# Kernel optimization log

Measured on AMD Instinct MI355X. Metric: run time of the kernel, lower is better.

The kernel has to match this reference:

```python
import jax, jax.numpy as jnp
import numpy as np

NUM_QUBITS = 8
QD = 2 ** NUM_QUBITS          # 256
PI = float(np.pi)
D_MODEL = 512
NUM_HEADS = 8
HEAD_DIM = D_MODEL // NUM_HEADS
LN_EPS = 1e-5


def _superposition(feat):
    # torch bug faithfully reproduced: state starts as e0 and is *multiplied*
    # by per-qubit amplitudes, so only index 0 survives. All values real.
    B, S, d = feat.shape
    idx = np.arange(NUM_QUBITS) % d
    theta = feat[:, :, idx] * PI                       # [B,S,nq]
    cos_h = jnp.cos(theta * 0.5)
    sin_h = jnp.sin(theta * 0.5)
    mask = (np.arange(QD)[None, :] >> np.arange(NUM_QUBITS)[:, None]) & 1  # [nq,QD]
    amps = jnp.where(mask[None, None] == 0, cos_h[..., None], sin_h[..., None])  # [B,S,nq,QD]
    prod = jnp.prod(amps, axis=2)                      # [B,S,QD]
    e0 = jnp.zeros((QD,), feat.dtype).at[0].set(1.0)
    state = prod * e0
    norm = jnp.sqrt(jnp.sum(state * state, axis=-1, keepdims=True))
    return state / (norm + 1e-10)


def _linear_entangle(ent):
    # entangle_matrix is block-diagonal with symmetric 2x2 blocks [[a,a],[a,-a]];
    # state @ M.T == pairwise 2x2 matmul (identical math, avoids 65536^2 matrix)
    B, S, D = ent.shape
    a = 0.7071
    M = jnp.array([[a, a], [a, -a]], ent.dtype)
    return (ent.reshape(B, S, D // 2, 2) @ M).reshape(B, S, D)


def _layer_norm(x, g, b):
    m = jnp.mean(x, axis=-1, keepdims=True)
    v = jnp.mean((x - m) ** 2, axis=-1, keepdims=True)
    return (x - m) * jax.lax.rsqrt(v + LN_EPS) * g + b


def setup_inputs() -> dict:
    key = jax.random.key(0)
    ks = jax.random.split(key, 16)
    D = D_MODEL
    s = 1.0 / np.sqrt(D)
    inp = {
        'audio_features': jax.random.normal(ks[0], (2, 256, D), jnp.float32),
        'visual_features': jax.random.normal(ks[1], (2, 256, D), jnp.float32),
        'Wq': jax.random.normal(ks[2], (D, D), jnp.float32) * s,
        'bq': jnp.zeros((D,), jnp.float32),
        'Wk': jax.random.normal(ks[3], (D, D), jnp.float32) * s,
        'bk': jnp.zeros((D,), jnp.float32),
        'Wv': jax.random.normal(ks[4], (D, D), jnp.float32) * s,
        'bv': jnp.zeros((D,), jnp.float32),
        'Wo': jax.random.normal(ks[5], (D, D), jnp.float32) * s,
        'bo': jnp.zeros((D,), jnp.float32),
        'We': jax.random.normal(ks[6], (D, D), jnp.float32) * s,
        'be': jnp.zeros((D,), jnp.float32),
        'gamma': jnp.ones((D,), jnp.float32),
        'beta': jnp.zeros((D,), jnp.float32),
    }
    return inp


def reference(audio_features, visual_features, Wq, bq, Wk, bk, Wv, bv,
              Wo, bo, We, be, gamma, beta):
    B, S, D = audio_features.shape
    H, hd = NUM_HEADS, HEAD_DIM

    aq = audio_features @ Wq + bq
    av = audio_features @ Wv + bv
    vk = visual_features @ Wk + bk
    vv = visual_features @ Wv + bv

    qa = _superposition(audio_features @ We + be)    # [B,S,QD]
    qv = _superposition(visual_features @ We + be)   # [B,S,QD]
    ent = (qa[..., :, None] * qv[..., None, :]).reshape(B, S, QD * QD)
    ent = _linear_entangle(ent)                      # [B,S,QD^2]

    probs = ent * ent
    qsum = jnp.sum(probs, axis=-1)                   # [B,S]
    ang = jnp.where(ent < 0, PI, 0.0)                # angle of a real number
    interference = jnp.cos(jnp.mean(ang, axis=-1))   # [B,S]
    scale = (qsum * interference)[:, None, :, None]  # [B,1,S,1]

    def heads(x):
        return x.reshape(B, S, H, hd).transpose(0, 2, 1, 3)

    aqh, vkh, vvh, avh = heads(aq), heads(vk), heads(vv), heads(av)
    logits = scale * jnp.einsum('bhqd,bhkd->bhqk', aqh, vkh) / np.sqrt(hd)
    attn = jax.nn.softmax(logits, axis=-1)           # [B,H,S,S]

    audio_att = jnp.einsum('bhqk,bhkd->bhqd', attn, vvh)
    visual_att = jnp.einsum('bhqk,bhqd->bhkd', attn, avh)
    audio_out = audio_att.transpose(0, 2, 1, 3).reshape(B, S, D) @ Wo + bo
    visual_out = visual_att.transpose(0, 2, 1, 3).reshape(B, S, D) @ Wo + bo

    audio_final = _layer_norm(audio_features + audio_out, gamma, beta)
    visual_final = _layer_norm(visual_features + visual_out, gamma, beta)

    quantum_coherence = jnp.mean(jnp.abs(ent))
    pn = probs / (jnp.sum(probs, axis=-1, keepdims=True) + 1e-10)
    entanglement_entropy = jnp.mean(-jnp.sum(pn * jnp.log(pn + 1e-10), axis=-1))

    return (audio_final, visual_final, quantum_coherence,
            entanglement_entropy, attn[:, -1])
```

## Files before the change

kernel.cpp:

```cpp
#include <hip/hip_runtime.h>
#include <math.h>

#define PI_F 3.14159265358979323846f

typedef __attribute__((ext_vector_type(8))) short short8v;
typedef __attribute__((ext_vector_type(4))) float f32x4;
typedef __attribute__((ext_vector_type(16))) float f32x16;

__device__ __forceinline__ unsigned short f2bf(float f) {
    unsigned int u = __float_as_uint(f);
    u += 0x7fffu + ((u >> 16) & 1u);
    return (unsigned short)(u >> 16);
}

__device__ __forceinline__ unsigned int cvtpk_bf16(float lo, float hi) {
    unsigned int r;
    asm("v_cvt_pk_bf16_f32 %0, %1, %2" : "=v"(r) : "v"(lo), "v"(hi));
    return r;
}

union W8 { unsigned int w[4]; short8v v; };

__device__ __forceinline__ void gload_lds16(const void* g, void* l) {
    __builtin_amdgcn_global_load_lds((const __attribute__((address_space(1))) unsigned int*)g,
                                     (__attribute__((address_space(3))) unsigned int*)l, 16, 0, 0);
}

__device__ __forceinline__ short8v pack8(const float* p) {
    float4 a0 = *(const float4*)(p);
    float4 a1 = *(const float4*)(p + 4);
    W8 u;
    u.w[0] = cvtpk_bf16(a0.x, a0.y);
    u.w[1] = cvtpk_bf16(a0.z, a0.w);
    u.w[2] = cvtpk_bf16(a1.x, a1.y);
    u.w[3] = cvtpk_bf16(a1.z, a1.w);
    return u.v;
}

__global__ __launch_bounds__(256) void prep_tok(const float* __restrict__ audio,
                                                const float* __restrict__ visual,
                                                const float* __restrict__ Wq,
                                                const float* __restrict__ Wk,
                                                const float* __restrict__ Wv,
                                                const float* __restrict__ Wo,
                                                const float* __restrict__ We,
                                                const float* __restrict__ be,
                                                unsigned short* __restrict__ audio_b,
                                                unsigned short* __restrict__ visual_b,
                                                unsigned short* __restrict__ Wqt,
                                                unsigned short* __restrict__ Wkt,
                                                unsigned short* __restrict__ Wvt,
                                                unsigned short* __restrict__ Wot,
                                                float* __restrict__ scale,
                                                float* __restrict__ coh_tok,
                                                float* __restrict__ ent_tok) {
    __shared__ float tile[32][33];
    const int bid = blockIdx.x;
    if (bid < 1536) {
        const int z = bid >> 8;
        const int x0 = (bid & 15) * 32, y0 = ((bid >> 4) & 15) * 32;
        const int tx = threadIdx.x & 31, ty = threadIdx.x >> 5;
        if (z < 2) {
            const float* src = z ? visual : audio;
            unsigned short* dst = z ? visual_b : audio_b;
#pragma unroll
            for (int i = 0; i < 4; i++) {
                int r = y0 + ty + i * 8;
                dst[r * 512 + x0 + tx] = f2bf(src[r * 512 + x0 + tx]);
            }
        } else {
            const float* src = (z == 2) ? Wq : (z == 3) ? Wk : (z == 4) ? Wv : Wo;
            unsigned short* dst = (z == 2) ? Wqt : (z == 3) ? Wkt : (z == 4) ? Wvt : Wot;
#pragma unroll
            for (int i = 0; i < 4; i++)
                tile[ty + i * 8][tx] = src[(y0 + ty + i * 8) * 512 + x0 + tx];
            __syncthreads();
#pragma unroll
            for (int i = 0; i < 4; i++) {
                int n = x0 + ty + i * 8;
                dst[n * 512 + y0 + tx] = f2bf(tile[tx][ty + i * 8]);
            }
        }
    } else {
        const int t = (bid - 1536) * 4 + (threadIdx.x >> 6);
        const int lane = threadIdx.x & 63;
        float accA[8] = {}, accV[8] = {};
#pragma unroll
        for (int i = 0; i < 8; i++) {
            int k = i * 64 + lane;
            float wa = audio[t * 512 + k], wv = visual[t * 512 + k];
            const float* wrow = &We[k * 512];
#pragma unroll
            for (int c = 0; c < 8; c++) {
                float w = wrow[c];
                accA[c] += wa * w;
                accV[c] += wv * w;
            }
        }
#pragma unroll
        for (int c = 0; c < 8; c++) {
#pragma unroll
            for (int o = 32; o >= 1; o >>= 1) {
                accA[c] += __shfl_xor(accA[c], o);
                accV[c] += __shfl_xor(accV[c], o);
            }
        }
        if (lane == 0) {
            float pa = 1.f, pv = 1.f;
#pragma unroll
            for (int c = 0; c < 8; c++) {
                pa *= cosf((accA[c] + be[c]) * (PI_F * 0.5f));
                pv *= cosf((accV[c] + be[c]) * (PI_F * 0.5f));
            }
            float s0a = pa / (fabsf(pa) + 1e-10f);
            float s0v = pv / (fabsf(pv) + 1e-10f);
            float e = s0a * s0v;
            const float a = 0.7071f;
            float ent0 = a * e;
            float qsum = 2.f * ent0 * ent0;
            float interf = (ent0 < 0.f) ? cosf(2.f * PI_F / 65536.f) : 1.f;
            scale[t] = qsum * interf;
            coh_tok[t] = 2.f * fabsf(ent0);
            float p = (ent0 * ent0) / (qsum + 1e-10f);
            ent_tok[t] = -2.f * p * logf(p + 1e-10f);
        }
    }
}

struct MfmaArgs {
    const unsigned short* A[4];
    const unsigned short* Bt[4];
    const float* bias[4];
    void* C[4];
    int obf[4];
};

__global__ __launch_bounds__(256) void gemm_mfma(MfmaArgs args) {
    const int zb = blockIdx.z;
    const unsigned short* __restrict__ A = args.A[zb];
    const unsigned short* __restrict__ Bt = args.Bt[zb];
    const float* __restrict__ bias = args.bias[zb];

    const int n0 = blockIdx.x * 64;
    const int m0 = blockIdx.y * 64;

    __shared__ unsigned short As[64 * 64];
    __shared__ unsigned short Bs[64 * 64];

    const int tid = threadIdx.x;
    const int lane = tid & 63;
    const int wid = tid >> 6;
    const int wr = wid >> 1, wc = wid & 1;
    const int l15 = lane & 15;
    const int lhi = lane >> 4;

    f32x4 acc[2][2] = {};

    for (int kt = 0; kt < 8; kt++) {
        const int k0 = kt * 64;
#pragma unroll
        for (int i = 0; i < 2; i++) {
            int row = i * 32 + wid * 8 + (lane >> 3);
            int pc = lane & 7;
            int lc = pc ^ (row & 7);
            const unsigned short* gA = A + (m0 + row) * 512 + k0 + lc * 8;
            const unsigned short* gB = Bt + (n0 + row) * 512 + k0 + lc * 8;
            gload_lds16(gA, (char*)As + i * 4096 + wid * 1024);
            gload_lds16(gB, (char*)Bs + i * 4096 + wid * 1024);
        }
        __syncthreads();
#pragma unroll
        for (int ks = 0; ks < 2; ks++) {
            short8v a[2], b[2];
            const int lcr = ks * 4 + lhi;
#pragma unroll
            for (int qi = 0; qi < 2; qi++) {
                int row = wr * 32 + qi * 16 + l15;
                int pcc = lcr ^ (row & 7);
                a[qi] = *(const short8v*)((const char*)As + row * 128 + pcc * 16);
            }
#pragma unroll
            for (int nj = 0; nj < 2; nj++) {
                int row = wc * 32 + nj * 16 + l15;
                int pcc = lcr ^ (row & 7);
                b[nj] = *(const short8v*)((const char*)Bs + row * 128 + pcc * 16);
            }
#pragma unroll
            for (int qi = 0; qi < 2; qi++)
#pragma unroll
                for (int nj = 0; nj < 2; nj++)
                    acc[qi][nj] = __builtin_amdgcn_mfma_f32_16x16x32_bf16(a[qi], b[nj], acc[qi][nj], 0, 0, 0);
        }
        __syncthreads();
    }

    if (args.obf[zb]) {
        unsigned short* __restrict__ Cb = (unsigned short*)args.C[zb];
#pragma unroll
        for (int qi = 0; qi < 2; qi++)
#pragma unroll
            for (int nj = 0; nj < 2; nj++)
#pragma unroll
                for (int r = 0; r < 4; r++) {
                    int row = m0 + wr * 32 + qi * 16 + lhi * 4 + r;
                    int col = n0 + wc * 32 + nj * 16 + l15;
                    Cb[row * 512 + col] = f2bf(acc[qi][nj][r] + bias[col]);
                }
    } else {
        float* __restrict__ C = (float*)args.C[zb];
#pragma unroll
        for (int qi = 0; qi < 2; qi++)
#pragma unroll
            for (int nj = 0; nj < 2; nj++)
#pragma unroll
                for (int r = 0; r < 4; r++) {
                    int row = m0 + wr * 32 + qi * 16 + lhi * 4 + r;
                    int col = n0 + wc * 32 + nj * 16 + l15;
                    C[row * 512 + col] = acc[qi][nj][r] + bias[col];
                }
    }
}

__global__ __launch_bounds__(512, 2) void attn_roles(const unsigned short* __restrict__ aqb,
                                                     const unsigned short* __restrict__ vkb,
                                                     const float* __restrict__ vv,
                                                     const float* __restrict__ av,
                                                     const float* __restrict__ scale,
                                                     const float* __restrict__ coh,
                                                     const float* __restrict__ entt,
                                                     unsigned short* __restrict__ attcat_b,
                                                     float* __restrict__ attn_last,
                                                     float* __restrict__ scal_out) {
    __shared__ char smem[65536];
    char* Kb = smem;
    char* VF = smem + 32768;

    const int tid = threadIdx.x;
    const int wid = tid >> 6;
    const int lane = tid & 63;
    const int lq = lane & 31;
    const int hi = lane >> 5;

    if (blockIdx.x == 8) {
        if (blockIdx.y || blockIdx.z) return;
        float c = coh[tid], e = entt[tid];
#pragma unroll
        for (int o = 32; o >= 1; o >>= 1) {
            c += __shfl_xor(c, o);
            e += __shfl_xor(e, o);
        }
        float* rc = (float*)smem;
        float* re = rc + 8;
        if (lane == 0) { rc[wid] = c; re[wid] = e; }
        __syncthreads();
        if (tid == 0) {
            float cs = 0.f, es = 0.f;
#pragma unroll
            for (int i = 0; i < 8; i++) { cs += rc[i]; es += re[i]; }
            scal_out[0] = cs / (512.f * 65536.f);
            scal_out[1] = es / 512.f;
        }
        return;
    }

    const int h = blockIdx.x, b = blockIdx.y, role = blockIdx.z;

    {
#pragma unroll
        for (int i = 0; i < 4; i++) {
            int r = wid * 32 + i * 8 + (lane >> 3);
            int lc = (lane & 7) ^ (r & 7);
            gload_lds16(vkb + (size_t)(b * 256 + r) * 512 + h * 64 + lc * 8,
                        Kb + wid * 4096 + i * 1024);
        }
    }

    if (role == 0) {
        const int t = wid;
#pragma unroll
        for (int si = 0; si < 2; si++) {
            const int s = hi + si * 2;
#pragma unroll
            for (int dt = 0; dt < 2; dt++) {
                const float* vb = vv + (size_t)(b * 256 + 32 * t + 8 * s) * 512 + h * 64 + 32 * dt + lq;
                W8 u;
                u.w[0] = cvtpk_bf16(vb[0 * 512], vb[1 * 512]);
                u.w[1] = cvtpk_bf16(vb[2 * 512], vb[3 * 512]);
                u.w[2] = cvtpk_bf16(vb[4 * 512], vb[5 * 512]);
                u.w[3] = cvtpk_bf16(vb[6 * 512], vb[7 * 512]);
                *(short8v*)(VF + ((((t * 4 + s) * 2 + dt) * 32 + lq) << 4)) = u.v;
            }
        }
    }
    __syncthreads();

    f32x16 p[8] = {};
    {
        short8v qf[4];
        const unsigned short* qbase = aqb + (size_t)(b * 256 + wid * 32 + lq) * 512 + h * 64;
#pragma unroll
        for (int s = 0; s < 4; s++) qf[s] = *(const short8v*)(qbase + (2 * s + hi) * 8);
#pragma unroll
        for (int t = 0; t < 8; t++) {
            const int krow = t * 32 + lq;
#pragma unroll
            for (int s = 0; s < 4; s++) {
                int slot = (2 * s + hi) ^ (krow & 7);
                short8v kf = *(const short8v*)(Kb + krow * 128 + (slot << 4));
                p[t] = __builtin_amdgcn_mfma_f32_32x32x16_bf16(kf, qf[s], p[t], 0, 0, 0);
            }
        }
    }

    {
        const float sq = scale[b * 256 + wid * 32 + lq] * 0.125f;
        float mx = -1e30f;
#pragma unroll
        for (int t = 0; t < 8; t++) {
            p[t] *= sq;
#pragma unroll
            for (int r = 0; r < 16; r++) mx = fmaxf(mx, p[t][r]);
        }
        mx = fmaxf(mx, __shfl_xor(mx, 32));
        float sum = 0.f;
#pragma unroll
        for (int t = 0; t < 8; t++)
#pragma unroll
            for (int r = 0; r < 16; r++) {
                float e = __expf(p[t][r] - mx);
                p[t][r] = e;
                sum += e;
            }
        sum += __shfl_xor(sum, 32);
        float inv = 1.0f / sum;
#pragma unroll
        for (int t = 0; t < 8; t++) p[t] *= inv;
    }

    if (role == 0) {
        f32x16 aacc[2] = {};
#pragma unroll
        for (int t = 0; t < 8; t++) {
            unsigned int c0 = cvtpk_bf16(p[t][0], p[t][1]);
            unsigned int c1 = cvtpk_bf16(p[t][2], p[t][3]);
            unsigned int c2 = cvtpk_bf16(p[t][4], p[t][5]);
            unsigned int c3 = cvtpk_bf16(p[t][6], p[t][7]);
            unsigned int e0 = (unsigned int)__shfl_xor((int)c0, 32);
            unsigned int e1 = (unsigned int)__shfl_xor((int)c1, 32);
            unsigned int e2 = (unsigned int)__shfl_xor((int)c2, 32);
            unsigned int e3 = (unsigned int)__shfl_xor((int)c3, 32);
            W8 fa0;
            fa0.w[0] = hi ? e2 : c0;
            fa0.w[1] = hi ? e3 : c1;
            fa0.w[2] = hi ? c2 : e0;
            fa0.w[3] = hi ? c3 : e1;
            unsigned int c4 = cvtpk_bf16(p[t][8], p[t][9]);
            unsigned int c5 = cvtpk_bf16(p[t][10], p[t][11]);
            unsigned int c6 = cvtpk_bf16(p[t][12], p[t][13]);
            unsigned int c7 = cvtpk_bf16(p[t][14], p[t][15]);
            unsigned int e4 = (unsigned int)__shfl_xor((int)c4, 32);
            unsigned int e5 = (unsigned int)__shfl_xor((int)c5, 32);
            unsigned int e6 = (unsigned int)__shfl_xor((int)c6, 32);
            unsigned int e7 = (unsigned int)__shfl_xor((int)c7, 32);
            W8 fa1;
            fa1.w[0] = hi ? e6 : c4;
            fa1.w[1] = hi ? e7 : c5;
            fa1.w[2] = hi ? c6 : e4;
            fa1.w[3] = hi ? c7 : e5;
#pragma unroll
            for (int dt = 0; dt < 2; dt++) {
                short8v vf = *(const short8v*)(VF + ((((t * 4 + hi) * 2 + dt) * 32 + lq) << 4));
                aacc[dt] = __builtin_amdgcn_mfma_f32_32x32x16_bf16(fa0.v, vf, aacc[dt], 0, 0, 0);
                short8v vg = *(const short8v*)(VF + ((((t * 4 + hi + 2) * 2 + dt) * 32 + lq) << 4));
                aacc[dt] = __builtin_amdgcn_mfma_f32_32x32x16_bf16(fa1.v, vg, aacc[dt], 0, 0, 0);
            }
        }
#pragma unroll
        for (int dt = 0; dt < 2; dt++)
#pragma unroll
            for (int r = 0; r < 16; r++) {
                int qrow = wid * 32 + (r & 3) + 8 * (r >> 2) + 4 * hi;
                attcat_b[(size_t)(b * 256 + qrow) * 512 + h * 64 + 32 * dt + lq] = f2bf(aacc[dt][r]);
            }
        __syncthreads();

        if (h == 7) {
            float* tile = (float*)smem + (size_t)wid * (32 * 33);
            const int q2 = lane >> 1, koff = (lane & 1) * 16;
#pragma unroll
            for (int t = 0; t < 8; t++) {
#pragma unroll
                for (int r = 0; r < 16; r++)
                    tile[lq * 33 + ((r & 3) + 8 * (r >> 2) + 4 * hi)] = p[t][r];
                __syncthreads();
                float* orow = attn_last + (size_t)(b * 256 + wid * 32 + q2) * 256 + 32 * t + koff;
#pragma unroll
                for (int j = 0; j < 16; j++) orow[j] = tile[q2 * 33 + koff + j];
                __syncthreads();
            }
        }
        return;
    }

    __syncthreads();

    {
#pragma unroll
        for (int mi = 0; mi < 2; mi++) {
            const int m = wid * 4 + hi + mi * 2;
#pragma unroll
            for (int dt = 0; dt < 2; dt++) {
                const float* ab = av + (size_t)(b * 256 + 8 * m) * 512 + h * 64 + 32 * dt + lq;
                W8 u;
                u.w[0] = cvtpk_bf16(ab[0 * 512], ab[1 * 512]);
                u.w[1] = cvtpk_bf16(ab[2 * 512], ab[3 * 512]);
                u.w[2] = cvtpk_bf16(ab[4 * 512], ab[5 * 512]);
                u.w[3] = cvtpk_bf16(ab[6 * 512], ab[7 * 512]);
                *(short8v*)(Kb + (((m * 2 + dt) * 32 + lq) << 4)) = u.v;
            }
        }
        if ((wid >> 1) == 0) {
            const int dq = (wid & 1) * 32 + lq;
#pragma unroll
            for (int t = 0; t < 8; t++)
#pragma unroll
                for (int r = 0; r < 16; r++) {
                    int k = 32 * t + (r & 3) + 8 * (r >> 2) + 4 * hi;
                    int slot = (dq >> 3) ^ ((k ^ (k >> 3)) & 7);
                    *(unsigned short*)(VF + k * 128 + slot * 16 + (dq & 7) * 2) = f2bf(p[t][r]);
                }
        }
    }
    __syncthreads();

    f32x16 vacc[2] = {};
    {
        const int krow = wid * 32 + lq;
        const int xr = (krow ^ (krow >> 3)) & 7;
#pragma unroll
        for (int c = 0; c < 4; c++) {
#pragma unroll
            for (int uc = 0; uc < 4; uc++) {
                int slot = (2 * uc + hi) ^ xr;
                short8v pa = *(const short8v*)(VF + krow * 128 + slot * 16);
                int m = 2 * (4 * c + uc) + hi;
#pragma unroll
                for (int dt = 0; dt < 2; dt++) {
                    short8v af = *(const short8v*)(Kb + (((m * 2 + dt) * 32 + lq) << 4));
                    vacc[dt] = __builtin_amdgcn_mfma_f32_32x32x16_bf16(pa, af, vacc[dt], 0, 0, 0);
                }
            }
            if (c < 3) {
                __syncthreads();
                if ((wid >> 1) == c + 1) {
                    const int dq = (wid & 1) * 32 + lq;
#pragma unroll
                    for (int t = 0; t < 8; t++)
#pragma unroll
                        for (int r = 0; r < 16; r++) {
                            int k = 32 * t + (r & 3) + 8 * (r >> 2) + 4 * hi;
                            int slot = (dq >> 3) ^ ((k ^ (k >> 3)) & 7);
                            *(unsigned short*)(VF + k * 128 + slot * 16 + (dq & 7) * 2) = f2bf(p[t][r]);
                        }
                }
                __syncthreads();
            }
        }
    }
#pragma unroll
    for (int dt = 0; dt < 2; dt++)
#pragma unroll
        for (int r = 0; r < 16; r++) {
            int krow = wid * 32 + (r & 3) + 8 * (r >> 2) + 4 * hi;
            attcat_b[(size_t)(512 + b * 256 + krow) * 512 + h * 64 + 32 * dt + lq] = f2bf(vacc[dt][r]);
        }
}

__global__ __launch_bounds__(256) void ln_final(const float* __restrict__ xa,
                                                const float* __restrict__ xv,
                                                const float* __restrict__ proj,
                                                const float* __restrict__ gamma,
                                                const float* __restrict__ beta,
                                                float* __restrict__ out) {
    __shared__ float red[4];
    const int t = blockIdx.x;
    const int tid = threadIdx.x;
    const int wid = tid >> 6, lane = tid & 63;

    const float* x = (t < 512) ? (xa + t * 512) : (xv + (t - 512) * 512);
    const float* pp = proj + t * 512;

    float y0 = x[tid] + pp[tid];
    float y1 = x[tid + 256] + pp[tid + 256];

    float s = y0 + y1;
#pragma unroll
    for (int o = 32; o >= 1; o >>= 1) s += __shfl_xor(s, o);
    if (lane == 0) red[wid] = s;
    __syncthreads();
    float mean = (red[0] + red[1] + red[2] + red[3]) * (1.f / 512.f);

    float d0 = y0 - mean, d1 = y1 - mean;
    float v = d0 * d0 + d1 * d1;
    __syncthreads();
#pragma unroll
    for (int o = 32; o >= 1; o >>= 1) v += __shfl_xor(v, o);
    if (lane == 0) red[wid] = v;
    __syncthreads();
    float var = (red[0] + red[1] + red[2] + red[3]) * (1.f / 512.f);
    float rstd = rsqrtf(var + 1e-5f);

    out[t * 512 + tid] = d0 * rstd * gamma[tid] + beta[tid];
    out[t * 512 + tid + 256] = d1 * rstd * gamma[tid + 256] + beta[tid + 256];
}

extern "C" void kernel_launch(void* const* d_in, const int* in_sizes, int n_in,
                              void* d_out, int out_size, void* d_ws, size_t ws_size,
                              hipStream_t stream) {
    const float* audio  = (const float*)d_in[0];
    const float* visual = (const float*)d_in[1];
    const float* Wq = (const float*)d_in[2];
    const float* bq = (const float*)d_in[3];
    const float* Wk = (const float*)d_in[4];
    const float* bk = (const float*)d_in[5];
    const float* Wv = (const float*)d_in[6];
    const float* bv = (const float*)d_in[7];
    const float* Wo = (const float*)d_in[8];
    const float* bo = (const float*)d_in[9];
    const float* We = (const float*)d_in[10];
    const float* be = (const float*)d_in[11];
    const float* gamma = (const float*)d_in[12];
    const float* beta  = (const float*)d_in[13];
    float* out = (float*)d_out;

    float* ws = (float*)d_ws;
    float* vv    = ws;
    float* av    = ws + 262144;
    float* proj  = ws + 524288;
    float* scale = ws + 1048576;
    float* coh   = ws + 1049088;
    float* entt  = ws + 1049600;
    unsigned short* attcat_b = (unsigned short*)(ws + 1050112);
    unsigned short* audio_b  = (unsigned short*)(ws + 1312256);
    unsigned short* visual_b = (unsigned short*)(ws + 1443328);
    unsigned short* Wqt  = (unsigned short*)(ws + 1574400);
    unsigned short* Wkt  = (unsigned short*)(ws + 1705472);
    unsigned short* Wvt  = (unsigned short*)(ws + 1836544);
    unsigned short* Wot  = (unsigned short*)(ws + 1967616);
    unsigned short* aq_b = (unsigned short*)(ws + 2098688);
    unsigned short* vk_b = (unsigned short*)(ws + 2229760);

    hipLaunchKernelGGL(prep_tok, dim3(1664), dim3(256), 0, stream,
                       audio, visual, Wq, Wk, Wv, Wo, We, be,
                       audio_b, visual_b, Wqt, Wkt, Wvt, Wot,
                       scale, coh, entt);

    MfmaArgs g1;
    g1.A[0] = audio_b;  g1.Bt[0] = Wqt; g1.bias[0] = bq; g1.C[0] = aq_b; g1.obf[0] = 1;
    g1.A[1] = visual_b; g1.Bt[1] = Wkt; g1.bias[1] = bk; g1.C[1] = vk_b; g1.obf[1] = 1;
    g1.A[2] = visual_b; g1.Bt[2] = Wvt; g1.bias[2] = bv; g1.C[2] = vv;   g1.obf[2] = 0;
    g1.A[3] = audio_b;  g1.Bt[3] = Wvt; g1.bias[3] = bv; g1.C[3] = av;   g1.obf[3] = 0;
    hipLaunchKernelGGL(gemm_mfma, dim3(8, 8, 4), dim3(256), 0, stream, g1);

    hipLaunchKernelGGL(attn_roles, dim3(9, 2, 2), dim3(512), 0, stream,
                       aq_b, vk_b, vv, av, scale, coh, entt,
                       attcat_b, out + 524290, out + 524288);

    MfmaArgs g2;
    for (int i = 0; i < 4; i++) {
        g2.A[i] = attcat_b; g2.Bt[i] = Wot; g2.bias[i] = bo; g2.C[i] = proj; g2.obf[i] = 0;
    }
    hipLaunchKernelGGL(gemm_mfma, dim3(8, 16, 1), dim3(256), 0, stream, g2);

    hipLaunchKernelGGL(ln_final, dim3(1024), dim3(256), 0, stream,
                       audio, visual, proj, gamma, beta, out);
}
```

Baseline: 52.86 us.

## Emit V projections as transposed bf16 and load them into LDS asynchronously

The V projection GEMMs now swap the MFMA operands so they write their outputs transposed (feature-major) in bf16 rather than fp32 row-major. The attention kernel can then stage V tiles into LDS with direct global-to-LDS 16-byte loads. This replaces the strided fp32 gathers and in-register bf16 conversion it did before. The change halves the V traffic and removes conversion work from attention, but the GEMM epilogue now does strided transposed bf16 stores, and the LDS layout must match what the later MFMA reads expect.

```diff
diff --git a/kernel.cpp b/kernel.cpp
--- a/kernel.cpp
+++ b/kernel.cpp
@@ -24,17 +24,6 @@
 __device__ __forceinline__ void gload_lds16(const void* g, void* l) {
     __builtin_amdgcn_global_load_lds((const __attribute__((address_space(1))) unsigned int*)g,
                                      (__attribute__((address_space(3))) unsigned int*)l, 16, 0, 0);
-}
-
-__device__ __forceinline__ short8v pack8(const float* p) {
-    float4 a0 = *(const float4*)(p);
-    float4 a1 = *(const float4*)(p + 4);
-    W8 u;
-    u.w[0] = cvtpk_bf16(a0.x, a0.y);
-    u.w[1] = cvtpk_bf16(a0.z, a0.w);
-    u.w[2] = cvtpk_bf16(a1.x, a1.y);
-    u.w[3] = cvtpk_bf16(a1.z, a1.w);
-    return u.v;
 }
 
 __global__ __launch_bounds__(256) void prep_tok(const float* __restrict__ audio,
@@ -133,6 +122,7 @@
     const float* bias[4];
     void* C[4];
     int obf[4];
+    int otr[4];
 };
 
 __global__ __launch_bounds__(256) void gemm_mfma(MfmaArgs args) {
@@ -140,6 +130,7 @@
     const unsigned short* __restrict__ A = args.A[zb];
     const unsigned short* __restrict__ Bt = args.Bt[zb];
     const float* __restrict__ bias = args.bias[zb];
+    const int otr = args.otr[zb];
 
     const int n0 = blockIdx.x * 64;
     const int m0 = blockIdx.y * 64;
@@ -185,16 +176,36 @@
                 int pcc = lcr ^ (row & 7);
                 b[nj] = *(const short8v*)((const char*)Bs + row * 128 + pcc * 16);
             }
-#pragma unroll
-            for (int qi = 0; qi < 2; qi++)
-#pragma unroll
-                for (int nj = 0; nj < 2; nj++)
-                    acc[qi][nj] = __builtin_amdgcn_mfma_f32_16x16x32_bf16(a[qi], b[nj], acc[qi][nj], 0, 0, 0);
+            if (otr) {
+#pragma unroll
+                for (int qi = 0; qi < 2; qi++)
+#pragma unroll
+                    for (int nj = 0; nj < 2; nj++)
+                        acc[qi][nj] = __builtin_amdgcn_mfma_f32_16x16x32_bf16(b[nj], a[qi], acc[qi][nj], 0, 0, 0);
+            } else {
+#pragma unroll
+                for (int qi = 0; qi < 2; qi++)
+#pragma unroll
+                    for (int nj = 0; nj < 2; nj++)
+                        acc[qi][nj] = __builtin_amdgcn_mfma_f32_16x16x32_bf16(a[qi], b[nj], acc[qi][nj], 0, 0, 0);
+            }
         }
         __syncthreads();
     }
 
-    if (args.obf[zb]) {
+    if (otr) {
+        unsigned short* __restrict__ Ct = (unsigned short*)args.C[zb];
+#pragma unroll
+        for (int qi = 0; qi < 2; qi++)
+#pragma unroll
+            for (int nj = 0; nj < 2; nj++)
+#pragma unroll
+                for (int r = 0; r < 4; r++) {
+                    int nrow = n0 + wc * 32 + nj * 16 + lhi * 4 + r;
+                    int tcol = m0 + wr * 32 + qi * 16 + l15;
+                    Ct[nrow * 512 + tcol] = f2bf(acc[qi][nj][r] + bias[nrow]);
+                }
+    } else if (args.obf[zb]) {
         unsigned short* __restrict__ Cb = (unsigned short*)args.C[zb];
 #pragma unroll
         for (int qi = 0; qi < 2; qi++)
@@ -223,8 +234,8 @@
 
 __global__ __launch_bounds__(512, 2) void attn_roles(const unsigned short* __restrict__ aqb,
                                                      const unsigned short* __restrict__ vkb,
-                                                     const float* __restrict__ vv,
-                                                     const float* __restrict__ av,
+                                                     const unsigned short* __restrict__ vvt,
+                                                     const unsigned short* __restrict__ avt,
                                                      const float* __restrict__ scale,
                                                      const float* __restrict__ coh,
                                                      const float* __restrict__ entt,
@@ -276,20 +287,10 @@
     }
 
     if (role == 0) {
-        const int t = wid;
-#pragma unroll
-        for (int si = 0; si < 2; si++) {
-            const int s = hi + si * 2;
-#pragma unroll
-            for (int dt = 0; dt < 2; dt++) {
-                const float* vb = vv + (size_t)(b * 256 + 32 * t + 8 * s) * 512 + h * 64 + 32 * dt + lq;
-                W8 u;
-                u.w[0] = cvtpk_bf16(vb[0 * 512], vb[1 * 512]);
-                u.w[1] = cvtpk_bf16(vb[2 * 512], vb[3 * 512]);
-                u.w[2] = cvtpk_bf16(vb[4 * 512], vb[5 * 512]);
-                u.w[3] = cvtpk_bf16(vb[6 * 512], vb[7 * 512]);
-                *(short8v*)(VF + ((((t * 4 + s) * 2 + dt) * 32 + lq) << 4)) = u.v;
-            }
+#pragma unroll
+        for (int i = 0; i < 4; i++) {
+            gload_lds16(vvt + (size_t)(h * 64 + 32 * hi + lq) * 512 + b * 256 + 32 * wid + 8 * i,
+                        VF + wid * 4096 + i * 1024);
         }
     }
     __syncthreads();
@@ -406,18 +407,9 @@
 
     {
 #pragma unroll
-        for (int mi = 0; mi < 2; mi++) {
-            const int m = wid * 4 + hi + mi * 2;
-#pragma unroll
-            for (int dt = 0; dt < 2; dt++) {
-                const float* ab = av + (size_t)(b * 256 + 8 * m) * 512 + h * 64 + 32 * dt + lq;
-                W8 u;
-                u.w[0] = cvtpk_bf16(ab[0 * 512], ab[1 * 512]);
-                u.w[1] = cvtpk_bf16(ab[2 * 512], ab[3 * 512]);
-                u.w[2] = cvtpk_bf16(ab[4 * 512], ab[5 * 512]);
-                u.w[3] = cvtpk_bf16(ab[6 * 512], ab[7 * 512]);
-                *(short8v*)(Kb + (((m * 2 + dt) * 32 + lq) << 4)) = u.v;
-            }
+        for (int i = 0; i < 4; i++) {
+            gload_lds16(avt + (size_t)(h * 64 + 32 * hi + lq) * 512 + b * 256 + 8 * (wid * 4 + i),
+                        Kb + wid * 4096 + i * 1024);
         }
         if ((wid >> 1) == 0) {
             const int dq = (wid & 1) * 32 + lq;
@@ -534,21 +526,21 @@
     float* out = (float*)d_out;
 
     float* ws = (float*)d_ws;
-    float* vv    = ws;
-    float* av    = ws + 262144;
-    float* proj  = ws + 524288;
-    float* scale = ws + 1048576;
-    float* coh   = ws + 1049088;
-    float* entt  = ws + 1049600;
-    unsigned short* attcat_b = (unsigned short*)(ws + 1050112);
-    unsigned short* audio_b  = (unsigned short*)(ws + 1312256);
-    unsigned short* visual_b = (unsigned short*)(ws + 1443328);
-    unsigned short* Wqt  = (unsigned short*)(ws + 1574400);
-    unsigned short* Wkt  = (unsigned short*)(ws + 1705472);
-    unsigned short* Wvt  = (unsigned short*)(ws + 1836544);
-    unsigned short* Wot  = (unsigned short*)(ws + 1967616);
-    unsigned short* aq_b = (unsigned short*)(ws + 2098688);
-    unsigned short* vk_b = (unsigned short*)(ws + 2229760);
+    float* proj  = ws;
+    float* scale = ws + 524288;
+    float* coh   = ws + 524800;
+    float* entt  = ws + 525312;
+    unsigned short* attcat_b = (unsigned short*)(ws + 525824);
+    unsigned short* audio_b  = (unsigned short*)(ws + 787968);
+    unsigned short* visual_b = (unsigned short*)(ws + 919040);
+    unsigned short* Wqt  = (unsigned short*)(ws + 1050112);
+    unsigned short* Wkt  = (unsigned short*)(ws + 1181184);
+    unsigned short* Wvt  = (unsigned short*)(ws + 1312256);
+    unsigned short* Wot  = (unsigned short*)(ws + 1443328);
+    unsigned short* aq_b = (unsigned short*)(ws + 1574400);
+    unsigned short* vk_b = (unsigned short*)(ws + 1705472);
+    unsigned short* vvt  = (unsigned short*)(ws + 1836544);
+    unsigned short* avt  = (unsigned short*)(ws + 1967616);
 
     hipLaunchKernelGGL(prep_tok, dim3(1664), dim3(256), 0, stream,
                        audio, visual, Wq, Wk, Wv, Wo, We, be,
@@ -556,19 +548,20 @@
                        scale, coh, entt);
 
     MfmaArgs g1;
-    g1.A[0] = audio_b;  g1.Bt[0] = Wqt; g1.bias[0] = bq; g1.C[0] = aq_b; g1.obf[0] = 1;
-    g1.A[1] = visual_b; g1.Bt[1] = Wkt; g1.bias[1] = bk; g1.C[1] = vk_b; g1.obf[1] = 1;
-    g1.A[2] = visual_b; g1.Bt[2] = Wvt; g1.bias[2] = bv; g1.C[2] = vv;   g1.obf[2] = 0;
-    g1.A[3] = audio_b;  g1.Bt[3] = Wvt; g1.bias[3] = bv; g1.C[3] = av;   g1.obf[3] = 0;
+    g1.A[0] = audio_b;  g1.Bt[0] = Wqt; g1.bias[0] = bq; g1.C[0] = aq_b; g1.obf[0] = 1; g1.otr[0] = 0;
+    g1.A[1] = visual_b; g1.Bt[1] = Wkt; g1.bias[1] = bk; g1.C[1] = vk_b; g1.obf[1] = 1; g1.otr[1] = 0;
+    g1.A[2] = visual_b; g1.Bt[2] = Wvt; g1.bias[2] = bv; g1.C[2] = vvt;  g1.obf[2] = 1; g1.otr[2] = 1;
+    g1.A[3] = audio_b;  g1.Bt[3] = Wvt; g1.bias[3] = bv; g1.C[3] = avt;  g1.obf[3] = 1; g1.otr[3] = 1;
     hipLaunchKernelGGL(gemm_mfma, dim3(8, 8, 4), dim3(256), 0, stream, g1);
 
     hipLaunchKernelGGL(attn_roles, dim3(9, 2, 2), dim3(512), 0, stream,
-                       aq_b, vk_b, vv, av, scale, coh, entt,
+                       aq_b, vk_b, vvt, avt, scale, coh, entt,
                        attcat_b, out + 524290, out + 524288);
 
     MfmaArgs g2;
     for (int i = 0; i < 4; i++) {
-        g2.A[i] = attcat_b; g2.Bt[i] = Wot; g2.bias[i] = bo; g2.C[i] = proj; g2.obf[i] = 0;
+        g2.A[i] = attcat_b; g2.Bt[i] = Wot; g2.bias[i] = bo; g2.C[i] = proj;
+        g2.obf[i] = 0; g2.otr[i] = 0;
     }
     hipLaunchKernelGGL(gemm_mfma, dim3(8, 16, 1), dim3(256), 0, stream, g2);
 
```

New measurement: 52.35 us. No clear change (-1.0%).
